# Kernel tuning notes

Hardware: AMD Instinct MI355X
Metric: run time of the kernel (lower is better)

Reference implementation:

```python
import jax, jax.numpy as jnp
import numpy as np

D = 768  # n_dim


def setup_inputs() -> dict:
    key = jax.random.key(0)
    ks = jax.random.split(key, 9)
    B, S = 4, 4096
    s = 0.02
    return {
        "x": jax.random.normal(ks[0], (B, S, D), dtype=jnp.float32),
        "Wq": jax.random.normal(ks[1], (D, D), dtype=jnp.float32) * s,
        "bq": jax.random.normal(ks[2], (D,), dtype=jnp.float32) * s,
        "Wk": jax.random.normal(ks[3], (D, D), dtype=jnp.float32) * s,
        "bk": jax.random.normal(ks[4], (D,), dtype=jnp.float32) * s,
        "Wv": jax.random.normal(ks[5], (D, D), dtype=jnp.float32) * s,
        "bv": jax.random.normal(ks[6], (D,), dtype=jnp.float32) * s,
        "Wc": jax.random.normal(ks[7], (D, D), dtype=jnp.float32) * s,
        "bc": jax.random.normal(ks[8], (D,), dtype=jnp.float32) * s,
    }


def reference(x, Wq, bq, Wk, bk, Wv, bv, Wc, bc):
    # Faithful to the source's executed math (its head-reshape and masked_fill
    # results are discarded): single-'head' full-dim attention, NO causal mask,
    # scale = n_dim**-0.5, then a transpose(1,2).reshape element permutation.
    B, S, nd = x.shape
    q = jnp.einsum('bsd,ed->bse', x, Wq) + bq  # nn.Linear: x @ W.T + b
    k = jnp.einsum('bsd,ed->bse', x, Wk) + bk
    v = jnp.einsum('bsd,ed->bse', x, Wv) + bv
    att = jnp.einsum('bqd,bkd->bqk', q, k) * (nd ** -0.5)  # [B,S,S]
    att = jax.nn.softmax(att, axis=-1)  # no mask (bug preserved)
    y = jnp.einsum('bqk,bkd->bqd', att, v)  # [B,S,D]
    y = jnp.transpose(y, (0, 2, 1)).reshape(B, S, nd)  # element permutation (bug preserved)
    return jnp.einsum('bsd,ed->bse', y, Wc) + bc
```

## Files before the change

kernel.cpp:

```cpp
#include <hip/hip_runtime.h>
#include <stdint.h>


typedef __bf16 bf16;
typedef __bf16 bf16x4 __attribute__((ext_vector_type(4)));
typedef __bf16 bf16x8 __attribute__((ext_vector_type(8)));
typedef float f32x4 __attribute__((ext_vector_type(4)));

#define OFF_Q    0L
#define OFF_K    25165824L
#define OFF_VT   50331648L
#define OFF_W    75497472L
#define OFF_B    80216064L
#define OFF_FLAG 80222208L
#define OFF_L    80223232L
#define OFF_ATT  80289792L
#define ATT_B    33554432L
#define SD       3145728L

#define M_PLAIN  0
#define M_TRANSC 1
#define M_EXPSUM 2
#define M_DIVL   3

__device__ __forceinline__ void glds16(const void* g, void* s) {
  __builtin_amdgcn_global_load_lds((const __attribute__((address_space(1))) void*)g,
                                   (__attribute__((address_space(3))) void*)s, 16, 0, 0);
}

__global__ void sniff_dtype(const uint16_t* __restrict__ x, int* __restrict__ flag)
{
  const int t = threadIdx.x;
  int bad = 0;
  for (int i = t; i < 4096; i += 256) {
    const int e = (x[2 * i] >> 7) & 0xFF;
    bad |= (e >= 0xE0);
  }
  __shared__ int s;
  if (t == 0) s = 0;
  __syncthreads();
  if (bad) s = 1;
  __syncthreads();
  if (t == 0) *flag = s;
}

__global__ void normalize8(const void* __restrict__ src, bf16* __restrict__ dst,
                           long n8, const int* __restrict__ flag)
{
  const long i = (long)blockIdx.x * 256 + threadIdx.x;
  if (i >= n8) return;
  bf16x8 o;
  if (*flag) {
    const float4 a = ((const float4*)src)[2 * i];
    const float4 b = ((const float4*)src)[2 * i + 1];
    o[0] = (bf16)a.x; o[1] = (bf16)a.y; o[2] = (bf16)a.z; o[3] = (bf16)a.w;
    o[4] = (bf16)b.x; o[5] = (bf16)b.y; o[6] = (bf16)b.z; o[7] = (bf16)b.w;
  } else {
    o = ((const bf16x8*)src)[i];
  }
  ((bf16x8*)dst)[i] = o;
}

__global__ void zero_f32(float* __restrict__ p)
{
  p[(long)blockIdx.x * 256 + threadIdx.x] = 0.f;
}

template <int MODE>
__launch_bounds__(256, 2)
__global__ void gemm_bt(const bf16* __restrict__ A, int lda, long strideA,
                        const bf16* __restrict__ Bm, int ldb, long strideB,
                        void* __restrict__ Cv, int ldc, long strideC,
                        int K, const bf16* __restrict__ bias, float alpha,
                        const int* __restrict__ oflag, float* __restrict__ lsum)
{
  __shared__ bf16 As[2 * 128 * 32];
  __shared__ bf16 Bs[2 * 128 * 32];
  A  += (long)blockIdx.z * strideA;
  Bm += (long)blockIdx.z * strideB;
  if (MODE == M_EXPSUM || MODE == M_DIVL) lsum += (long)blockIdx.z * 4096L;
  const int tid = threadIdx.x;
  const int wave = tid >> 6, lane = tid & 63;
  const int lr = lane & 15, quad = lane >> 4;
  const int wm = (wave >> 1) * 64, wn = (wave & 1) * 64;
  const long m0 = (long)blockIdx.y * 128, n0 = (long)blockIdx.x * 128;

  f32x4 acc[4][4];
  const f32x4 zero = {0.f, 0.f, 0.f, 0.f};
#pragma unroll
  for (int i = 0; i < 4; ++i)
#pragma unroll
    for (int j = 0; j < 4; ++j) acc[i][j] = zero;

  const int r0 = tid >> 2, c0 = (tid & 3) * 8;
  const bf16* pA0 = A + (m0 + r0) * (long)lda + c0;
  const bf16* pA1 = A + (m0 + 64 + r0) * (long)lda + c0;
  const bf16* pB0 = Bm + (n0 + r0) * (long)ldb + c0;
  const bf16* pB1 = Bm + (n0 + 64 + r0) * (long)ldb + c0;
  bf16* sA0 = As + wave * 512;
  bf16* sA1 = As + 2048 + wave * 512;
  bf16* sB0 = Bs + wave * 512;
  bf16* sB1 = Bs + 2048 + wave * 512;

  for (int k0 = 0; k0 < K; k0 += 64) {
    __syncthreads();
    glds16(pA0 + k0, sA0);
    glds16(pA1 + k0, sA1);
    glds16(pB0 + k0, sB0);
    glds16(pB1 + k0, sB1);
    glds16(pA0 + k0 + 32, sA0 + 4096);
    glds16(pA1 + k0 + 32, sA1 + 4096);
    glds16(pB0 + k0 + 32, sB0 + 4096);
    glds16(pB1 + k0 + 32, sB1 + 4096);
    __syncthreads();
#pragma unroll
    for (int s = 0; s < 2; ++s) {
      bf16x8 aF[4], bF[4];
#pragma unroll
      for (int i = 0; i < 4; ++i) {
        aF[i] = *(const bf16x8*)(As + s * 4096 + (wm + i * 16 + lr) * 32 + quad * 8);
        bF[i] = *(const bf16x8*)(Bs + s * 4096 + (wn + i * 16 + lr) * 32 + quad * 8);
      }
#pragma unroll
      for (int i = 0; i < 4; ++i)
#pragma unroll
        for (int j = 0; j < 4; ++j) {
          if (MODE == M_TRANSC)
            acc[i][j] = __builtin_amdgcn_mfma_f32_16x16x32_bf16(aF[i], bF[j], acc[i][j], 0, 0, 0);
          else
            acc[i][j] = __builtin_amdgcn_mfma_f32_16x16x32_bf16(bF[j], aF[i], acc[i][j], 0, 0, 0);
        }
    }
  }

  if (MODE == M_TRANSC) {
#pragma unroll
    for (int j = 0; j < 4; ++j) {
      const long col = n0 + wn + j * 16 + lr;
      const float bv = (float)bias[col];
#pragma unroll
      for (int i = 0; i < 4; ++i) {
        const long row = m0 + wm + i * 16 + quad * 4;
        bf16x4 v4;
#pragma unroll
        for (int r = 0; r < 4; ++r) v4[r] = (bf16)((acc[i][j][r] + bv) * alpha);
        *(bf16x4*)((bf16*)Cv + (long)blockIdx.z * strideC + col * (long)ldc + row) = v4;
      }
    }
    return;
  }

  const int outf32 = (MODE == M_PLAIN) && (oflag != nullptr) && (*oflag != 0);
  long colb[4];
  f32x4 addv[4];
#pragma unroll
  for (int j = 0; j < 4; ++j) {
    colb[j] = n0 + wn + j * 16 + quad * 4;
    if (MODE == M_PLAIN) {
      const bf16x4 bb = *(const bf16x4*)(bias + colb[j]);
#pragma unroll
      for (int r = 0; r < 4; ++r) addv[j][r] = (float)bb[r];
    } else if (MODE == M_DIVL) {
      const f32x4 lv = *(const f32x4*)(lsum + colb[j]);
#pragma unroll
      for (int r = 0; r < 4; ++r) addv[j][r] = 1.0f / lv[r];
    }
  }
#pragma unroll
  for (int i = 0; i < 4; ++i) {
    const long row = m0 + wm + i * 16 + lr;
    char* rowp = (char*)Cv + ((long)blockIdx.z * strideC + row * (long)ldc) * (outf32 ? 4 : 2);
    float rsum = 0.f;
#pragma unroll
    for (int j = 0; j < 4; ++j) {
      f32x4 v;
#pragma unroll
      for (int r = 0; r < 4; ++r) {
        float t = acc[i][j][r];
        if (MODE == M_PLAIN)       t = (t + addv[j][r]) * alpha;
        else if (MODE == M_EXPSUM) t = __expf(t);
        else if (MODE == M_DIVL)   t = t * addv[j][r];
        v[r] = t;
      }
      if (MODE == M_PLAIN && outf32) {
        *(f32x4*)(rowp + colb[j] * 4) = v;
      } else {
        bf16x4 v4;
#pragma unroll
        for (int r = 0; r < 4; ++r) v4[r] = (bf16)v[r];
        if (MODE == M_EXPSUM) {
#pragma unroll
          for (int r = 0; r < 4; ++r) rsum += (float)v4[r];
        }
        *(bf16x4*)(rowp + colb[j] * 2) = v4;
      }
    }
    if (MODE == M_EXPSUM) {
      rsum += __shfl_xor(rsum, 16);
      rsum += __shfl_xor(rsum, 32);
      if (quad == 0) atomicAdd(&lsum[row], rsum);
    }
  }
}

extern "C" void kernel_launch(void* const* d_in, const int* in_sizes, int n_in,
                              void* d_out, int out_size, void* d_ws, size_t ws_size,
                              hipStream_t stream)
{
  (void)in_sizes; (void)n_in; (void)out_size;
  char* ws = (char*)d_ws;

  if (ws_size < (size_t)(OFF_ATT + ATT_B)) return;
  const size_t avail = ws_size - (size_t)OFF_ATT;
  int group = (int)(avail / (size_t)ATT_B);
  group = group >= 4 ? 4 : (group >= 2 ? 2 : 1);

  bf16*  q    = (bf16*)(ws + OFF_Q);
  bf16*  k    = (bf16*)(ws + OFF_K);
  bf16*  vT2  = (bf16*)(ws + OFF_VT);
  bf16*  Wn   = (bf16*)(ws + OFF_W);
  bf16*  bn   = (bf16*)(ws + OFF_B);
  int*   flg  = (int*)(ws + OFF_FLAG);
  float* lbase= (float*)(ws + OFF_L);
  bf16*  att  = (bf16*)(ws + OFF_ATT);
  bf16*  xn   = att;

  dim3 blk(256, 1, 1);
  const float qs = 0.03608439182435161f;

  sniff_dtype<<<1, blk, 0, stream>>>((const uint16_t*)d_in[0], flg);
  normalize8<<<6144, blk, 0, stream>>>(d_in[0], xn, 1572864L, flg);
  for (int w = 0; w < 4; ++w) {
    normalize8<<<288, blk, 0, stream>>>(d_in[1 + 2 * w], Wn + w * 589824L, 73728L, flg);
    normalize8<<<1, blk, 0, stream>>>(d_in[2 + 2 * w], bn + w * 768L, 96L, flg);
  }
  zero_f32<<<64, blk, 0, stream>>>(lbase);

  dim3 gproj(6, 128, 1);
  gemm_bt<M_PLAIN><<<gproj, blk, 0, stream>>>(xn, 768, 0, Wn + 0 * 589824L, 768, 0,
                                              q, 768, 0, 768, bn + 0, qs, nullptr, nullptr);
  gemm_bt<M_PLAIN><<<gproj, blk, 0, stream>>>(xn, 768, 0, Wn + 1 * 589824L, 768, 0,
                                              k, 768, 0, 768, bn + 768, 1.f, nullptr, nullptr);
  gemm_bt<M_TRANSC><<<gproj, blk, 0, stream>>>(xn, 768, 0, Wn + 2 * 589824L, 768, 0,
                                               vT2, 16384, 0, 768, bn + 1536, 1.f, nullptr, nullptr);

  for (int g = 0; g < 4; g += group) {
    dim3 gs(32, 32, group);
    gemm_bt<M_EXPSUM><<<gs, blk, 0, stream>>>(q + g * SD, 768, SD, k + g * SD, 768, SD,
                                              att, 4096, 16777216L, 768, nullptr, 1.f,
                                              nullptr, lbase + g * 4096L);
    dim3 gpv(32, 6, group);
    gemm_bt<M_DIVL><<<gpv, blk, 0, stream>>>(vT2 + g * 4096L, 16384, 4096L,
                                             att, 4096, 16777216L,
                                             q + g * SD, 4096, SD, 4096, nullptr, 1.f,
                                             nullptr, lbase + g * 4096L);
  }

  dim3 gout(6, 128, 1);
  gemm_bt<M_PLAIN><<<gout, blk, 0, stream>>>(q, 768, 0, Wn + 3 * 589824L, 768, 0,
                                             d_out, 768, 0, 768, bn + 2304, 1.f, flg, nullptr);
}
```

Baseline: 540.6 us.

## Replace 128x128 GEMM with 256x256 tiled, swizzled, double-buffered pipelined kernel

Replaces the 128x128-tile, 256-thread GEMM with a 256x256-tile, 512-thread kernel. It uses XOR-swizzled LDS layout, double-buffered global-to-LDS prefetch interleaved with MFMA phases, s_setprio, and an XCD-aware block remapping. It also fuses the normalization and zeroing launches into one kernel. The aim is more operand reuse per LDS load, less bank conflicting, and load latency hidden behind compute, at the cost of higher register pressure and fewer blocks per grid (e.g. 192 blocks for projections).

```diff
diff --git a/kernel.cpp b/kernel.cpp
--- a/kernel.cpp
+++ b/kernel.cpp
@@ -28,6 +28,21 @@
                                    (__attribute__((address_space(3))) void*)s, 16, 0, 0);
 }
 
+#define SBAR()  do { asm volatile("" ::: "memory"); __builtin_amdgcn_s_barrier(); \
+                     asm volatile("" ::: "memory"); } while (0)
+#define LGKM0() do { asm volatile("s_waitcnt lgkmcnt(0)" ::: "memory"); \
+                     __builtin_amdgcn_sched_barrier(0); } while (0)
+
+#define MFMA_AB(ac, aa, bb) do { \
+  if (MODE == M_TRANSC) { \
+    ac = __builtin_amdgcn_mfma_f32_16x16x32_bf16((aa)[0], (bb)[0], ac, 0, 0, 0); \
+    ac = __builtin_amdgcn_mfma_f32_16x16x32_bf16((aa)[1], (bb)[1], ac, 0, 0, 0); \
+  } else { \
+    ac = __builtin_amdgcn_mfma_f32_16x16x32_bf16((bb)[0], (aa)[0], ac, 0, 0, 0); \
+    ac = __builtin_amdgcn_mfma_f32_16x16x32_bf16((bb)[1], (aa)[1], ac, 0, 0, 0); \
+  } \
+} while (0)
+
 __global__ void sniff_dtype(const uint16_t* __restrict__ x, int* __restrict__ flag)
 {
   const int t = threadIdx.x;
@@ -44,13 +59,12 @@
   if (t == 0) *flag = s;
 }
 
-__global__ void normalize8(const void* __restrict__ src, bf16* __restrict__ dst,
-                           long n8, const int* __restrict__ flag)
-{
-  const long i = (long)blockIdx.x * 256 + threadIdx.x;
+__device__ __forceinline__ void norm8(const void* __restrict__ src, bf16* __restrict__ dst,
+                                      long i, long n8, int f)
+{
   if (i >= n8) return;
   bf16x8 o;
-  if (*flag) {
+  if (f) {
     const float4 a = ((const float4*)src)[2 * i];
     const float4 b = ((const float4*)src)[2 * i + 1];
     o[0] = (bf16)a.x; o[1] = (bf16)a.y; o[2] = (bf16)a.z; o[3] = (bf16)a.w;
@@ -61,76 +75,163 @@
   ((bf16x8*)dst)[i] = o;
 }
 
-__global__ void zero_f32(float* __restrict__ p)
-{
-  p[(long)blockIdx.x * 256 + threadIdx.x] = 0.f;
+__global__ void normalize_all(const void* x,
+                              const void* w0, const void* b0, const void* w1, const void* b1,
+                              const void* w2, const void* b2, const void* w3, const void* b3,
+                              bf16* __restrict__ xn, bf16* __restrict__ Wn,
+                              bf16* __restrict__ bn, float* __restrict__ lsum,
+                              const int* __restrict__ flag)
+{
+  const int t = threadIdx.x;
+  const int f = *flag;
+  int b = blockIdx.x;
+  if (b < 6144) { norm8(x, xn, (long)b * 256 + t, 1572864L, f); return; }
+  b -= 6144;
+  if (b < 1152) {
+    const int w = b / 288;
+    const void* s = (w == 0) ? w0 : (w == 1) ? w1 : (w == 2) ? w2 : w3;
+    norm8(s, Wn + (long)w * 589824L, (long)(b % 288) * 256 + t, 73728L, f);
+    return;
+  }
+  b -= 1152;
+  if (b < 4) {
+    const void* s = (b == 0) ? b0 : (b == 1) ? b1 : (b == 2) ? b2 : b3;
+    norm8(s, bn + (long)b * 768L, (long)t, 96L, f);
+    return;
+  }
+  b -= 4;
+  lsum[(long)b * 256 + t] = 0.f;
 }
 
 template <int MODE>
-__launch_bounds__(256, 2)
-__global__ void gemm_bt(const bf16* __restrict__ A, int lda, long strideA,
+__launch_bounds__(512, 2)
+__global__ void gemm256(const bf16* __restrict__ A, int lda, long strideA,
                         const bf16* __restrict__ Bm, int ldb, long strideB,
                         void* __restrict__ Cv, int ldc, long strideC,
                         int K, const bf16* __restrict__ bias, float alpha,
                         const int* __restrict__ oflag, float* __restrict__ lsum)
 {
-  __shared__ bf16 As[2 * 128 * 32];
-  __shared__ bf16 Bs[2 * 128 * 32];
+  __shared__ bf16 lds[65536];
   A  += (long)blockIdx.z * strideA;
   Bm += (long)blockIdx.z * strideB;
   if (MODE == M_EXPSUM || MODE == M_DIVL) lsum += (long)blockIdx.z * 4096L;
+
+  const int gx = gridDim.x;
+  int lin = blockIdx.y * gx + blockIdx.x;
+  const int cpx = (gx * gridDim.y) >> 3;
+  lin = (lin & 7) * cpx + (lin >> 3);
+  const long m0 = (long)(lin / gx) * 256, n0 = (long)(lin % gx) * 256;
+
   const int tid = threadIdx.x;
-  const int wave = tid >> 6, lane = tid & 63;
+  const int wv = tid >> 6, lane = tid & 63;
   const int lr = lane & 15, quad = lane >> 4;
-  const int wm = (wave >> 1) * 64, wn = (wave & 1) * 64;
-  const long m0 = (long)blockIdx.y * 128, n0 = (long)blockIdx.x * 128;
-
-  f32x4 acc[4][4];
+  const int wm = (wv >> 2) << 7;
+  const int wn = (wv & 3) << 6;
+
+  f32x4 acc[8][4];
   const f32x4 zero = {0.f, 0.f, 0.f, 0.f};
 #pragma unroll
-  for (int i = 0; i < 4; ++i)
+  for (int i = 0; i < 8; ++i)
 #pragma unroll
     for (int j = 0; j < 4; ++j) acc[i][j] = zero;
 
-  const int r0 = tid >> 2, c0 = (tid & 3) * 8;
-  const bf16* pA0 = A + (m0 + r0) * (long)lda + c0;
-  const bf16* pA1 = A + (m0 + 64 + r0) * (long)lda + c0;
-  const bf16* pB0 = Bm + (n0 + r0) * (long)ldb + c0;
-  const bf16* pB1 = Bm + (n0 + 64 + r0) * (long)ldb + c0;
-  bf16* sA0 = As + wave * 512;
-  bf16* sA1 = As + 2048 + wave * 512;
-  bf16* sB0 = Bs + wave * 512;
-  bf16* sB1 = Bs + 2048 + wave * 512;
-
-  for (int k0 = 0; k0 < K; k0 += 64) {
-    __syncthreads();
-    glds16(pA0 + k0, sA0);
-    glds16(pA1 + k0, sA1);
-    glds16(pB0 + k0, sB0);
-    glds16(pB1 + k0, sB1);
-    glds16(pA0 + k0 + 32, sA0 + 4096);
-    glds16(pA1 + k0 + 32, sA1 + 4096);
-    glds16(pB0 + k0 + 32, sB0 + 4096);
-    glds16(pB1 + k0 + 32, sB1 + 4096);
-    __syncthreads();
-#pragma unroll
-    for (int s = 0; s < 2; ++s) {
-      bf16x8 aF[4], bF[4];
-#pragma unroll
-      for (int i = 0; i < 4; ++i) {
-        aF[i] = *(const bf16x8*)(As + s * 4096 + (wm + i * 16 + lr) * 32 + quad * 8);
-        bF[i] = *(const bf16x8*)(Bs + s * 4096 + (wn + i * 16 + lr) * 32 + quad * 8);
-      }
-#pragma unroll
-      for (int i = 0; i < 4; ++i)
-#pragma unroll
-        for (int j = 0; j < 4; ++j) {
-          if (MODE == M_TRANSC)
-            acc[i][j] = __builtin_amdgcn_mfma_f32_16x16x32_bf16(aF[i], bF[j], acc[i][j], 0, 0, 0);
-          else
-            acc[i][j] = __builtin_amdgcn_mfma_f32_16x16x32_bf16(bF[j], aF[i], acc[i][j], 0, 0, 0);
-        }
-    }
+  const int rowid = (wv << 4) + (lane >> 3);
+  const int colsw = ((lane & 7) ^ ((lane >> 3) & 7)) << 3;
+  const long lda8 = 8L * lda, ldb8 = 8L * ldb;
+  const bf16* paL = A + (m0 + rowid) * (long)lda + colsw;
+  const bf16* paH = paL + 128L * lda;
+  const bf16* pbL = Bm + (n0 + rowid) * (long)ldb + colsw;
+  const bf16* pbH = pbL + 128L * ldb;
+
+  auto STG = [&](const bf16* src, long ld8, int tbuf, int reg) {
+    bf16* d = lds + (tbuf << 15) + (reg << 13) + (wv << 10);
+    glds16(src, d);
+    glds16(src + ld8, d + 512);
+  };
+
+  const int regA = 1 + ((wv >> 2) << 1);
+  const int regB = wv & 2;
+  const int aoff = lr << 6;
+  const int boff = ((wv & 1) << 12) + (lr << 6);
+  const int xo  = (lr & 7) << 3;
+  const int ok0 = (quad << 3) ^ xo;
+  const int ok1 = (32 + (quad << 3)) ^ xo;
+
+  const int nt = K >> 6;
+
+  STG(pbL, ldb8, 0, 0); STG(paL, lda8, 0, 1);
+  STG(pbH, ldb8, 0, 2); STG(paH, lda8, 0, 3);
+  asm volatile("s_waitcnt vmcnt(4)" ::: "memory");
+  STG(pbL + 64, ldb8, 1, 0); STG(paL + 64, lda8, 1, 1);
+  STG(pbH + 64, ldb8, 1, 2);
+  asm volatile("s_waitcnt vmcnt(6)" ::: "memory");
+  SBAR();
+
+  for (int t = 0; t < nt; ++t) {
+    const int buf = t & 1;
+    const long k64 = (long)t << 6;
+    const bf16* LA = lds + (buf << 15) + (regA << 13) + aoff;
+    const bf16* LB = lds + (buf << 15) + (regB << 13) + boff;
+    bf16x8 aL[4][2], aH[4][2], bF[4][2];
+
+#pragma unroll
+    for (int i = 0; i < 4; ++i) {
+      aL[i][0] = *(const bf16x8*)(LA + i * 1024 + ok0);
+      aL[i][1] = *(const bf16x8*)(LA + i * 1024 + ok1);
+    }
+#pragma unroll
+    for (int j = 0; j < 4; ++j) {
+      bF[j][0] = *(const bf16x8*)(LB + j * 1024 + ok0);
+      bF[j][1] = *(const bf16x8*)(LB + j * 1024 + ok1);
+    }
+    if (t + 1 < nt) STG(paH + k64 + 64, lda8, (t + 1) & 1, 3);
+    SBAR();
+    LGKM0();
+    __builtin_amdgcn_s_setprio(1);
+#pragma unroll
+    for (int i = 0; i < 4; ++i)
+#pragma unroll
+      for (int j = 0; j < 2; ++j) MFMA_AB(acc[i][j], aL[i], bF[j]);
+    __builtin_amdgcn_s_setprio(0);
+    SBAR();
+
+#pragma unroll
+    for (int i = 0; i < 4; ++i) {
+      aH[i][0] = *(const bf16x8*)(LA + (4 + i) * 1024 + ok0);
+      aH[i][1] = *(const bf16x8*)(LA + (4 + i) * 1024 + ok1);
+    }
+    if (t + 2 < nt) STG(pbL + k64 + 128, ldb8, buf, 0);
+    SBAR();
+    LGKM0();
+    __builtin_amdgcn_s_setprio(1);
+#pragma unroll
+    for (int i = 0; i < 4; ++i)
+#pragma unroll
+      for (int j = 0; j < 2; ++j) MFMA_AB(acc[4 + i][j], aH[i], bF[j]);
+    __builtin_amdgcn_s_setprio(0);
+    SBAR();
+
+    if (t + 2 < nt) STG(paL + k64 + 128, lda8, buf, 1);
+    SBAR();
+    __builtin_amdgcn_s_setprio(1);
+#pragma unroll
+    for (int i = 0; i < 4; ++i)
+#pragma unroll
+      for (int j = 0; j < 2; ++j) MFMA_AB(acc[i][2 + j], aL[i], bF[2 + j]);
+    __builtin_amdgcn_s_setprio(0);
+    SBAR();
+
+    if (t + 2 < nt) STG(pbH + k64 + 128, ldb8, buf, 2);
+    SBAR();
+    __builtin_amdgcn_s_setprio(1);
+#pragma unroll
+    for (int i = 0; i < 4; ++i)
+#pragma unroll
+      for (int j = 0; j < 2; ++j) MFMA_AB(acc[4 + i][2 + j], aH[i], bF[2 + j]);
+    __builtin_amdgcn_s_setprio(0);
+    if (t + 2 < nt) asm volatile("s_waitcnt vmcnt(6)" ::: "memory");
+    else            asm volatile("s_waitcnt vmcnt(0)" ::: "memory");
+    SBAR();
   }
 
   if (MODE == M_TRANSC) {
@@ -139,7 +240,7 @@
       const long col = n0 + wn + j * 16 + lr;
       const float bv = (float)bias[col];
 #pragma unroll
-      for (int i = 0; i < 4; ++i) {
+      for (int i = 0; i < 8; ++i) {
         const long row = m0 + wm + i * 16 + quad * 4;
         bf16x4 v4;
 #pragma unroll
@@ -167,7 +268,7 @@
     }
   }
 #pragma unroll
-  for (int i = 0; i < 4; ++i) {
+  for (int i = 0; i < 8; ++i) {
     const long row = m0 + wm + i * 16 + lr;
     char* rowp = (char*)Cv + ((long)blockIdx.z * strideC + row * (long)ldc) * (outf32 ? 4 : 2);
     float rsum = 0.f;
@@ -225,38 +326,36 @@
   bf16*  att  = (bf16*)(ws + OFF_ATT);
   bf16*  xn   = att;
 
-  dim3 blk(256, 1, 1);
+  dim3 blk(256, 1, 1), blk2(512, 1, 1);
   const float qs = 0.03608439182435161f;
 
   sniff_dtype<<<1, blk, 0, stream>>>((const uint16_t*)d_in[0], flg);
-  normalize8<<<6144, blk, 0, stream>>>(d_in[0], xn, 1572864L, flg);
-  for (int w = 0; w < 4; ++w) {
-    normalize8<<<288, blk, 0, stream>>>(d_in[1 + 2 * w], Wn + w * 589824L, 73728L, flg);
-    normalize8<<<1, blk, 0, stream>>>(d_in[2 + 2 * w], bn + w * 768L, 96L, flg);
-  }
-  zero_f32<<<64, blk, 0, stream>>>(lbase);
-
-  dim3 gproj(6, 128, 1);
-  gemm_bt<M_PLAIN><<<gproj, blk, 0, stream>>>(xn, 768, 0, Wn + 0 * 589824L, 768, 0,
-                                              q, 768, 0, 768, bn + 0, qs, nullptr, nullptr);
-  gemm_bt<M_PLAIN><<<gproj, blk, 0, stream>>>(xn, 768, 0, Wn + 1 * 589824L, 768, 0,
-                                              k, 768, 0, 768, bn + 768, 1.f, nullptr, nullptr);
-  gemm_bt<M_TRANSC><<<gproj, blk, 0, stream>>>(xn, 768, 0, Wn + 2 * 589824L, 768, 0,
-                                               vT2, 16384, 0, 768, bn + 1536, 1.f, nullptr, nullptr);
+  normalize_all<<<7364, blk, 0, stream>>>(d_in[0],
+                                          d_in[1], d_in[2], d_in[3], d_in[4],
+                                          d_in[5], d_in[6], d_in[7], d_in[8],
+                                          xn, Wn, bn, lbase, flg);
+
+  dim3 gproj(3, 64, 1);
+  gemm256<M_PLAIN><<<gproj, blk2, 0, stream>>>(xn, 768, 0, Wn + 0 * 589824L, 768, 0,
+                                               q, 768, 0, 768, bn + 0, qs, nullptr, nullptr);
+  gemm256<M_PLAIN><<<gproj, blk2, 0, stream>>>(xn, 768, 0, Wn + 1 * 589824L, 768, 0,
+                                               k, 768, 0, 768, bn + 768, 1.f, nullptr, nullptr);
+  gemm256<M_TRANSC><<<gproj, blk2, 0, stream>>>(xn, 768, 0, Wn + 2 * 589824L, 768, 0,
+                                                vT2, 16384, 0, 768, bn + 1536, 1.f, nullptr, nullptr);
 
   for (int g = 0; g < 4; g += group) {
-    dim3 gs(32, 32, group);
-    gemm_bt<M_EXPSUM><<<gs, blk, 0, stream>>>(q + g * SD, 768, SD, k + g * SD, 768, SD,
-                                              att, 4096, 16777216L, 768, nullptr, 1.f,
+    dim3 gs(16, 16, group);
+    gemm256<M_EXPSUM><<<gs, blk2, 0, stream>>>(q + g * SD, 768, SD, k + g * SD, 768, SD,
+                                               att, 4096, 16777216L, 768, nullptr, 1.f,
+                                               nullptr, lbase + g * 4096L);
+    dim3 gpv(16, 3, group);
+    gemm256<M_DIVL><<<gpv, blk2, 0, stream>>>(vT2 + g * 4096L, 16384, 4096L,
+                                              att, 4096, 16777216L,
+                                              q + g * SD, 4096, SD, 4096, nullptr, 1.f,
                                               nullptr, lbase + g * 4096L);
-    dim3 gpv(32, 6, group);
-    gemm_bt<M_DIVL><<<gpv, blk, 0, stream>>>(vT2 + g * 4096L, 16384, 4096L,
-                                             att, 4096, 16777216L,
-                                             q + g * SD, 4096, SD, 4096, nullptr, 1.f,
-                                             nullptr, lbase + g * 4096L);
-  }
-
-  dim3 gout(6, 128, 1);
-  gemm_bt<M_PLAIN><<<gout, blk, 0, stream>>>(q, 768, 0, Wn + 3 * 589824L, 768, 0,
-                                             d_out, 768, 0, 768, bn + 2304, 1.f, flg, nullptr);
-}
+  }
+
+  dim3 gout(3, 64, 1);
+  gemm256<M_PLAIN><<<gout, blk2, 0, stream>>>(q, 768, 0, Wn + 3 * 589824L, 768, 0,
+                                              d_out, 768, 0, 768, bn + 2304, 1.f, flg, nullptr);
+}
```

After: 486.5 us. -10.0%, faster.
